# Optimization experiments

Measured on AMD Instinct MI355X. Metric: run time of the kernel, lower is better.

## Reference

```python
import jax, jax.numpy as jnp
import numpy as np

N, C, T, V, D = 64, 64, 256, 25, 64
BN_EPS = 1e-5


def _make_shift(v, ch, sign):
    idx = np.empty(v * ch, dtype=np.int64)
    for i in range(v):
        for j in range(ch):
            idx[i * ch + j] = (i * ch + j + sign * j * ch) % (ch * v)
    return jnp.asarray(idx, dtype=jnp.int32)


def setup_inputs() -> dict:
    key = jax.random.key(0)
    ks = jax.random.split(key, 8)
    return {
        "x0": jax.random.normal(ks[0], (N, C, T, V), dtype=jnp.float32),
        "fc1_w": jax.random.normal(ks[1], (C // 4, C), dtype=jnp.float32) * (1.0 / np.sqrt(C)),
        "fc1_b": jnp.zeros((C // 4,), dtype=jnp.float32),
        "fc2_w": jax.random.normal(ks[2], (4, C // 4), dtype=jnp.float32) * (1.0 / np.sqrt(C // 4)),
        "fc2_b": jnp.zeros((4,), dtype=jnp.float32),
        "Linear_weight": jax.random.normal(ks[3], (4, C, D), dtype=jnp.float32) * np.sqrt(1.0 / D),
        "Linear_bias": jax.random.normal(ks[4], (4, D), dtype=jnp.float32) * 0.02,
        "Feature_Mask": jax.random.normal(ks[5], (1, V, C), dtype=jnp.float32) * 0.1,
        "bn_gamma": 1.0 + 0.05 * jax.random.normal(ks[6], (V * D,), dtype=jnp.float32),
        "bn_beta": 0.05 * jax.random.normal(ks[7], (V * D,), dtype=jnp.float32),
        "shift_in": _make_shift(V, C, +1),
        "shift_out": _make_shift(V, D, -1),
        "epoch": 100,
    }


def reference(x0, fc1_w, fc1_b, fc2_w, fc2_b, Linear_weight, Linear_bias,
              Feature_Mask, bn_gamma, bn_beta, shift_in, shift_out, epoch):
    n, c, t, v = x0.shape
    d = Linear_weight.shape[-1]

    # DY_SEModule gate: global avg pool -> 1x1 convs -> tempered softmax over 4
    pooled = x0.mean(axis=(2, 3))                       # [n, c]
    h = jax.nn.relu(pooled @ fc1_w.T + fc1_b)           # [n, c//4]
    logits = h @ fc2_w.T + fc2_b                        # [n, 4]
    tao = (-(30.0 - 1.0) / 60.0 * epoch + 30.0) if epoch < 60 else 1.0
    gate = jax.nn.softmax(logits / tao, axis=1)         # [n, 4]

    # per-sample fused weights / bias
    W_fuse = jnp.einsum('kcd,nk->ncd', Linear_weight, gate)   # [n, c, d]
    b_fuse = jnp.einsum('kc,nk->nc', Linear_bias, gate)       # [n, d]

    # shift-in gather over flattened (v*c) channel axis
    x = x0.transpose(0, 2, 3, 1).reshape(n * t, v * c)  # [n*t, v*c]
    x = x[:, shift_in].reshape(n * t, v, c)
    x = x * (jnp.tanh(Feature_Mask) + 1.0)              # learnable feature mask
    x = x.reshape(n, t, v, c)

    # per-sample dynamic linear + bias
    x = jnp.einsum('ntvc,ncd->ntvd', x, W_fuse) + b_fuse[:, None, None, :]

    # shift-out gather
    x = x.reshape(n * t, v * d)[:, shift_out]           # [n*t, v*d]

    # BatchNorm1d (training mode: batch statistics over n*t)
    mean = x.mean(axis=0)
    var = jnp.var(x, axis=0)
    x = (x - mean) * jax.lax.rsqrt(var + BN_EPS) * bn_gamma + bn_beta

    x = x.reshape(n, t, v, d).transpose(0, 3, 1, 2)     # [n, d, t, v]
    return jax.nn.relu(x + x0)                          # identity residual (c == d)
```

## Files before the change

### kernel.cpp

```cpp
#include <hip/hip_runtime.h>
#include <hip/hip_bf16.h>
#include <math.h>

#define NN 64
#define CC 64
#define TT 256
#define VV 25
#define DD 64
#define BN_EPS 1e-5f

typedef short bf16x8 __attribute__((ext_vector_type(8)));
typedef float f32x4 __attribute__((ext_vector_type(4)));

#define WS_POOLED 0
#define WS_GATE   4096
#define WS_BFUSE  4352
#define WS_MASK   8448
#define WS_A      10048
#define WS_B      11648
#define WS_S1     13248
#define WS_S2     26048
#define WS_WTB    38848

#define OFF_W     0
#define OFF_MASK  9216
#define OFF_A     15728
#define OFF_B     22336
#define OFF_XM    28944
#define LDS_BYTES 54560

static __device__ __forceinline__ unsigned short f2bf(float x) {
    __hip_bfloat16 h = __float2bfloat16(x);
    return *(unsigned short*)&h;
}

__global__ __launch_bounds__(256) void k_pool(const float* __restrict__ x0,
                                              float* __restrict__ pooled) {
    __shared__ float red[256];
    const int bid = blockIdx.x;
    const float4* p = (const float4*)(x0 + (size_t)bid * (TT * VV));
    float s = 0.f;
    for (int k = threadIdx.x; k < (TT * VV) / 4; k += 256) {
        float4 v = p[k];
        s += v.x + v.y + v.z + v.w;
    }
    red[threadIdx.x] = s;
    __syncthreads();
    for (int off = 128; off > 0; off >>= 1) {
        if (threadIdx.x < off) red[threadIdx.x] += red[threadIdx.x + off];
        __syncthreads();
    }
    if (threadIdx.x == 0) pooled[bid] = red[0] * (1.f / (TT * VV));
}

__global__ __launch_bounds__(256) void k_gate(const float* __restrict__ fc1_w,
                                              const float* __restrict__ fc1_b,
                                              const float* __restrict__ fc2_w,
                                              const float* __restrict__ fc2_b,
                                              const float* __restrict__ lin_b,
                                              const float* __restrict__ fmask,
                                              const int* __restrict__ epoch_p,
                                              float* ws) {
    const int tid = threadIdx.x;
    float* pooled = ws + WS_POOLED;
    float* gate   = ws + WS_GATE;
    float* bfuse  = ws + WS_BFUSE;
    float* mask   = ws + WS_MASK;

    if (tid < 64) {
        const int n = tid;
        const float* po = pooled + n * 64;
        float h[16];
        for (int q = 0; q < 16; q++) {
            float z = fc1_b[q];
            for (int j = 0; j < 64; j++) z = fmaf(fc1_w[q * 64 + j], po[j], z);
            h[q] = fmaxf(z, 0.f);
        }
        float lg[4];
        for (int k = 0; k < 4; k++) {
            float z = fc2_b[k];
            for (int q = 0; q < 16; q++) z = fmaf(fc2_w[k * 16 + q], h[q], z);
            lg[k] = z;
        }
        const int ep = epoch_p[0];
        const float tao = (ep < 60) ? (-(29.0f / 60.0f) * (float)ep + 30.0f) : 1.0f;
        float mx = -1e30f;
        for (int k = 0; k < 4; k++) { lg[k] /= tao; mx = fmaxf(mx, lg[k]); }
        float se = 0.f;
        for (int k = 0; k < 4; k++) { lg[k] = expf(lg[k] - mx); se += lg[k]; }
        const float inv = 1.f / se;
        for (int k = 0; k < 4; k++) gate[n * 4 + k] = lg[k] * inv;
    }
    __syncthreads();
    for (int f = tid; f < 4096; f += 256) {
        const int n = f >> 6, d = f & 63;
        float s = 0.f;
        for (int k = 0; k < 4; k++) s = fmaf(lin_b[k * 64 + d], gate[n * 4 + k], s);
        bfuse[f] = s;
    }
    for (int f = tid; f < VV * CC; f += 256) mask[f] = tanhf(fmask[f]) + 1.0f;
}

__global__ __launch_bounds__(256) void k_wfuse(const float* __restrict__ lw, float* ws) {
    __shared__ float tile[64 * 65];
    const float* gate = ws + WS_GATE;
    unsigned short* wtb = (unsigned short*)(ws + WS_WTB);
    const int n = blockIdx.x;
    float g[4];
    for (int k = 0; k < 4; k++) g[k] = gate[n * 4 + k];
    for (int f = threadIdx.x; f < 4096; f += 256) {
        const int c = f >> 6, d = f & 63;
        float v = g[0] * lw[f] + g[1] * lw[4096 + f] + g[2] * lw[8192 + f] + g[3] * lw[12288 + f];
        tile[d * 65 + c] = v;
    }
    __syncthreads();
    for (int f = threadIdx.x; f < 4096; f += 256) {
        const int d = f >> 6, c = f & 63;
        wtb[n * 4096 + f] = f2bf(tile[d * 65 + c]);
    }
}

__global__ __launch_bounds__(256) void k_finalize(const float* __restrict__ gamma,
                                                  const float* __restrict__ beta,
                                                  float* ws) {
    const int f = blockIdx.x * 256 + threadIdx.x;
    if (f >= VV * DD) return;
    const int v = f >> 6, d = f & 63;
    const int vi = (v - d + 175) % 25;
    const int fin = vi * 64 + d;
    float s1 = 0.f, s2 = 0.f;
    for (int rep = 0; rep < 8; rep++) {
        s1 += ws[WS_S1 + rep * 1600 + fin];
        s2 += ws[WS_S2 + rep * 1600 + fin];
    }
    const float mean = s1 * (1.f / (NN * TT));
    float var = s2 * (1.f / (NN * TT)) - mean * mean;
    var = fmaxf(var, 0.f);
    const float rs = rsqrtf(var + BN_EPS);
    const float a = gamma[f] * rs;
    ws[WS_A + f] = a;
    ws[WS_B + f] = beta[f] - mean * a;
}

template <int PHASE>
__global__ __launch_bounds__(256) void k_main(const float* __restrict__ x0,
                                              const unsigned short* __restrict__ wtb,
                                              const float* __restrict__ ws,
                                              float* __restrict__ wsmut,
                                              float* __restrict__ out) {
    __shared__ __align__(16) char pool[LDS_BYTES];
    unsigned short (*Wl)[72] = (unsigned short(*)[72])(pool + OFF_W);
    float* maskL = (float*)(pool + OFF_MASK);
    float* Al = (float*)(pool + OFF_A);
    float* Bl = (float*)(pool + OFF_B);
    unsigned short (*Xm)[72] = (unsigned short(*)[72])(pool + OFF_XM);
    float* outl = (float*)(pool + OFF_XM);

    const int n = blockIdx.y, tb = blockIdx.x;
    const int tid = threadIdx.x;
    const int wv = tid >> 6, lane = tid & 63;
    const int lrow = lane & 15, lgrp = lane >> 4;
    const int dcol = wv * 16 + lrow;

    {
        const uint4* wsrc = (const uint4*)(wtb + n * 4096);
        for (int it = tid; it < 512; it += 256) {
            uint4 u = wsrc[it];
            const int f8 = it * 8;
            *(uint4*)&Wl[f8 >> 6][f8 & 63] = u;
        }
        const float* maskf = ws + WS_MASK;
        for (int f = tid; f < 1600; f += 256) {
            const int i = f >> 6, j = f & 63;
            maskL[i * 65 + j] = maskf[f];
        }
        if (PHASE == 0) {
            float* z = (float*)(pool + OFF_A);
            for (int f = tid; f < 3304; f += 256) z[f] = 0.f;
        } else {
            const float* Ag = ws + WS_A;
            const float* Bg = ws + WS_B;
            for (int f = tid; f < 1600; f += 256) {
                const int v = f >> 6, d = f & 63;
                Al[v * 66 + d] = Ag[f];
                Bl[v * 66 + d] = Bg[f];
            }
        }
    }
    const float bfv = ws[WS_BFUSE + n * 64 + dcol];
    __syncthreads();

    const bf16x8 b0 = *(const bf16x8*)&Wl[dcol][8 * lgrp];
    const bf16x8 b1 = *(const bf16x8*)&Wl[dcol][32 + 8 * lgrp];

    float s1r[7][4], s2r[7][4];
    if (PHASE == 0) {
#pragma unroll
        for (int m = 0; m < 7; m++)
#pragma unroll
            for (int r = 0; r < 4; r++) { s1r[m][r] = 0.f; s2r[m][r] = 0.f; }
    }

    const size_t nbase = (size_t)n * (CC * TT * VV);

    for (int ck = 0; ck < 4; ck++) {
        const int gcol0 = tb * 400 + ck * 100;
        for (int l4 = tid; l4 < 1600; l4 += 256) {
            const int j = l4 / 25, q = l4 - j * 25;
            const float4 xv = *(const float4*)(x0 + nbase + j * 6400 + gcol0 + q * 4);
            int jm = j; if (jm >= 50) jm -= 50; else if (jm >= 25) jm -= 25;
            const int r0 = q * 4;
            const float xe[4] = {xv.x, xv.y, xv.z, xv.w};
#pragma unroll
            for (int e = 0; e < 4; e++) {
                const int r = r0 + e;
                const int trel = (r >= 75) ? 3 : (r >= 50) ? 2 : (r >= 25) ? 1 : 0;
                const int p = r - trel * 25;
                int i = p - jm + 25; if (i >= 25) i -= 25;
                Xm[trel * 25 + i][j] = f2bf(xe[e] * maskL[i * 65 + j]);
            }
        }
        __syncthreads();
        f32x4 acc[7];
#pragma unroll
        for (int m = 0; m < 7; m++) {
            f32x4 a = {bfv, bfv, bfv, bfv};
            const bf16x8 a0 = *(const bf16x8*)&Xm[m * 16 + lrow][8 * lgrp];
            const bf16x8 a1 = *(const bf16x8*)&Xm[m * 16 + lrow][32 + 8 * lgrp];
            a = __builtin_amdgcn_mfma_f32_16x16x32_bf16(a0, b0, a, 0, 0, 0);
            a = __builtin_amdgcn_mfma_f32_16x16x32_bf16(a1, b1, a, 0, 0, 0);
            acc[m] = a;
        }
        __syncthreads();

        if (PHASE == 0) {
#pragma unroll
            for (int m = 0; m < 7; m++) {
#pragma unroll
                for (int r = 0; r < 4; r++) {
                    const int row = m * 16 + 4 * lgrp + r;
                    if (row < 100) {
                        const float y = acc[m][r];
                        s1r[m][r] += y;
                        s2r[m][r] = fmaf(y, y, s2r[m][r]);
                    }
                }
            }
        } else {
#pragma unroll
            for (int m = 0; m < 7; m++) {
#pragma unroll
                for (int r = 0; r < 4; r++) {
                    const int row = m * 16 + 4 * lgrp + r;
                    if (row < 100) {
                        const int trel = (row >= 75) ? 3 : (row >= 50) ? 2 : (row >= 25) ? 1 : 0;
                        const int v = row - trel * 25;
                        int vo = v + dcol;
                        if (vo >= 75) vo -= 75; else if (vo >= 50) vo -= 50; else if (vo >= 25) vo -= 25;
                        outl[dcol * 100 + trel * 25 + vo] =
                            fmaf(Al[vo * 66 + dcol], acc[m][r], Bl[vo * 66 + dcol]);
                    }
                }
            }
            __syncthreads();
            for (int l4 = tid; l4 < 1600; l4 += 256) {
                const int dd = l4 / 25, q = l4 - dd * 25;
                const float4 vv = *(const float4*)&outl[dd * 100 + q * 4];
                const float4 xr = *(const float4*)(x0 + nbase + dd * 6400 + gcol0 + q * 4);
                float4 o;
                o.x = fmaxf(vv.x + xr.x, 0.f);
                o.y = fmaxf(vv.y + xr.y, 0.f);
                o.z = fmaxf(vv.z + xr.z, 0.f);
                o.w = fmaxf(vv.w + xr.w, 0.f);
                *(float4*)(out + nbase + dd * 6400 + gcol0 + q * 4) = o;
            }
            __syncthreads();
        }
    }

    if (PHASE == 0) {
        float* s1l = Al;
        float* s2l = Bl;
#pragma unroll
        for (int m = 0; m < 7; m++) {
#pragma unroll
            for (int r = 0; r < 4; r++) {
                const int row = m * 16 + 4 * lgrp + r;
                if (row < 100) {
                    int v = row;
                    if (v >= 75) v -= 75; else if (v >= 50) v -= 50; else if (v >= 25) v -= 25;
                    __hip_atomic_fetch_add(&s1l[v * 66 + dcol], s1r[m][r],
                                           __ATOMIC_RELAXED, __HIP_MEMORY_SCOPE_WORKGROUP);
                    __hip_atomic_fetch_add(&s2l[v * 66 + dcol], s2r[m][r],
                                           __ATOMIC_RELAXED, __HIP_MEMORY_SCOPE_WORKGROUP);
                }
            }
        }
        __syncthreads();
        float* g1 = wsmut + WS_S1 + (n & 7) * 1600;
        float* g2 = wsmut + WS_S2 + (n & 7) * 1600;
        for (int f = tid; f < 1600; f += 256) {
            const int v = f >> 6, d = f & 63;
            atomicAdd(&g1[f], s1l[v * 66 + d]);
            atomicAdd(&g2[f], s2l[v * 66 + d]);
        }
    }
}

extern "C" void kernel_launch(void* const* d_in, const int* in_sizes, int n_in,
                              void* d_out, int out_size, void* d_ws, size_t ws_size,
                              hipStream_t stream) {
    const float* x0    = (const float*)d_in[0];
    const float* fc1_w = (const float*)d_in[1];
    const float* fc1_b = (const float*)d_in[2];
    const float* fc2_w = (const float*)d_in[3];
    const float* fc2_b = (const float*)d_in[4];
    const float* lw    = (const float*)d_in[5];
    const float* lb    = (const float*)d_in[6];
    const float* fmask = (const float*)d_in[7];
    const float* gamma = (const float*)d_in[8];
    const float* beta  = (const float*)d_in[9];
    const int* epoch   = (const int*)d_in[12];
    float* ws  = (float*)d_ws;
    float* out = (float*)d_out;
    const unsigned short* wtb = (const unsigned short*)(ws + WS_WTB);

    k_pool<<<NN * CC, 256, 0, stream>>>(x0, ws + WS_POOLED);
    k_gate<<<1, 256, 0, stream>>>(fc1_w, fc1_b, fc2_w, fc2_b, lb, fmask, epoch, ws);
    k_wfuse<<<NN, 256, 0, stream>>>(lw, ws);
    hipMemsetAsync((char*)d_ws + WS_S1 * sizeof(float), 0, 25600 * sizeof(float), stream);

    dim3 g2(16, 64);
    k_main<0><<<g2, 256, 0, stream>>>(x0, wtb, ws, ws, out);
    k_finalize<<<7, 256, 0, stream>>>(gamma, beta, ws);
    k_main<1><<<g2, 256, 0, stream>>>(x0, wtb, ws, ws, out);
}
```

Before: 230.4 us.

## Shrink LDS, double phase-1 grid, write output directly from MFMA registers

Phase 1 now computes the transposed MFMA product (W as A operand) and writes the normalized, residual-added output straight from registers instead of staging through LDS, which drops two barriers per chunk. BN scale and shift are packed as a bf16 pair in one word, LDS is sized per phase with a launch bound of 4 blocks per CU, phase 1 uses twice as many blocks, and atomic stat replicas grow from 8 to 16. The goals are higher occupancy, less LDS traffic and sync, and less atomic contention. The costs are bf16 rounding of the BN scale and shift, and scattered, uncoalesced scalar global loads and stores in the epilogue.

```diff
diff --git a/kernel.cpp b/kernel.cpp
--- a/kernel.cpp
+++ b/kernel.cpp
@@ -8,6 +8,7 @@
 #define VV 25
 #define DD 64
 #define BN_EPS 1e-5f
+#define NREP 16
 
 typedef short bf16x8 __attribute__((ext_vector_type(8)));
 typedef float f32x4 __attribute__((ext_vector_type(4)));
@@ -16,18 +17,10 @@
 #define WS_GATE   4096
 #define WS_BFUSE  4352
 #define WS_MASK   8448
-#define WS_A      10048
-#define WS_B      11648
+#define WS_ABP    10048
 #define WS_S1     13248
-#define WS_S2     26048
-#define WS_WTB    38848
-
-#define OFF_W     0
-#define OFF_MASK  9216
-#define OFF_A     15728
-#define OFF_B     22336
-#define OFF_XM    28944
-#define LDS_BYTES 54560
+#define WS_S2     38848
+#define WS_WTB    64448
 
 static __device__ __forceinline__ unsigned short f2bf(float x) {
     __hip_bfloat16 h = __float2bfloat16(x);
@@ -129,7 +122,7 @@
     const int vi = (v - d + 175) % 25;
     const int fin = vi * 64 + d;
     float s1 = 0.f, s2 = 0.f;
-    for (int rep = 0; rep < 8; rep++) {
+    for (int rep = 0; rep < NREP; rep++) {
         s1 += ws[WS_S1 + rep * 1600 + fin];
         s2 += ws[WS_S2 + rep * 1600 + fin];
     }
@@ -138,29 +131,32 @@
     var = fmaxf(var, 0.f);
     const float rs = rsqrtf(var + BN_EPS);
     const float a = gamma[f] * rs;
-    ws[WS_A + f] = a;
-    ws[WS_B + f] = beta[f] - mean * a;
+    const float b = beta[f] - mean * a;
+    const unsigned pa = (unsigned)f2bf(a);
+    const unsigned pb = (unsigned)f2bf(b);
+    ((unsigned*)ws)[WS_ABP + f] = pa | (pb << 16);
 }
 
 template <int PHASE>
-__global__ __launch_bounds__(256) void k_main(const float* __restrict__ x0,
-                                              const unsigned short* __restrict__ wtb,
-                                              const float* __restrict__ ws,
-                                              float* __restrict__ wsmut,
-                                              float* __restrict__ out) {
-    __shared__ __align__(16) char pool[LDS_BYTES];
-    unsigned short (*Wl)[72] = (unsigned short(*)[72])(pool + OFF_W);
-    float* maskL = (float*)(pool + OFF_MASK);
-    float* Al = (float*)(pool + OFF_A);
-    float* Bl = (float*)(pool + OFF_B);
-    unsigned short (*Xm)[72] = (unsigned short(*)[72])(pool + OFF_XM);
-    float* outl = (float*)(pool + OFF_XM);
+__global__ __launch_bounds__(256, 4) void k_main(const float* __restrict__ x0,
+                                                 const unsigned short* __restrict__ wtb,
+                                                 const float* __restrict__ ws,
+                                                 float* __restrict__ wsmut,
+                                                 float* __restrict__ out) {
+    constexpr int LDSZ = (PHASE == 0) ? 31856 : 38656;
+    __shared__ __align__(16) char pool[LDSZ];
+    unsigned short (*Wl)[72] = (unsigned short(*)[72])(pool);
+    float* maskL = (float*)(pool + 9216);
+    unsigned short (*Xm)[72] = (unsigned short(*)[72])(pool + 15728);
+    unsigned* ABl = (unsigned*)(pool + 31856);
 
     const int n = blockIdx.y, tb = blockIdx.x;
     const int tid = threadIdx.x;
     const int wv = tid >> 6, lane = tid & 63;
     const int lrow = lane & 15, lgrp = lane >> 4;
     const int dcol = wv * 16 + lrow;
+    constexpr int NCK = (PHASE == 0) ? 4 : 2;
+    const int colbase = tb * 100 * NCK;
 
     {
         const uint4* wsrc = (const uint4*)(wtb + n * 4096);
@@ -169,29 +165,25 @@
             const int f8 = it * 8;
             *(uint4*)&Wl[f8 >> 6][f8 & 63] = u;
         }
-        const float* maskf = ws + WS_MASK;
-        for (int f = tid; f < 1600; f += 256) {
-            const int i = f >> 6, j = f & 63;
-            maskL[i * 65 + j] = maskf[f];
-        }
-        if (PHASE == 0) {
-            float* z = (float*)(pool + OFF_A);
-            for (int f = tid; f < 3304; f += 256) z[f] = 0.f;
-        } else {
-            const float* Ag = ws + WS_A;
-            const float* Bg = ws + WS_B;
-            for (int f = tid; f < 1600; f += 256) {
-                const int v = f >> 6, d = f & 63;
-                Al[v * 66 + d] = Ag[f];
-                Bl[v * 66 + d] = Bg[f];
-            }
+        for (int f = tid; f < 1600; f += 256)
+            maskL[(f >> 6) * 65 + (f & 63)] = ws[WS_MASK + f];
+        for (int f = tid; f < 864; f += 256) ((unsigned short*)Xm)[7200 + f] = 0;
+        if (PHASE == 1) {
+            const unsigned* abp = (const unsigned*)(ws + WS_ABP);
+            for (int f = tid; f < 1600; f += 256)
+                ABl[(f >> 6) * 68 + (f & 63)] = abp[f];
         }
     }
     const float bfv = ws[WS_BFUSE + n * 64 + dcol];
+    f32x4 bias4;
+    if (PHASE == 1) {
+        const float4 b4 = *(const float4*)&ws[WS_BFUSE + n * 64 + wv * 16 + 4 * lgrp];
+        bias4[0] = b4.x; bias4[1] = b4.y; bias4[2] = b4.z; bias4[3] = b4.w;
+    }
     __syncthreads();
 
-    const bf16x8 b0 = *(const bf16x8*)&Wl[dcol][8 * lgrp];
-    const bf16x8 b1 = *(const bf16x8*)&Wl[dcol][32 + 8 * lgrp];
+    const bf16x8 w0 = *(const bf16x8*)&Wl[dcol][8 * lgrp];
+    const bf16x8 w1 = *(const bf16x8*)&Wl[dcol][32 + 8 * lgrp];
 
     float s1r[7][4], s2r[7][4];
     if (PHASE == 0) {
@@ -203,84 +195,86 @@
 
     const size_t nbase = (size_t)n * (CC * TT * VV);
 
-    for (int ck = 0; ck < 4; ck++) {
-        const int gcol0 = tb * 400 + ck * 100;
+    for (int ck = 0; ck < NCK; ck++) {
+        const int gcol0 = colbase + ck * 100;
+        if (ck) __syncthreads();
         for (int l4 = tid; l4 < 1600; l4 += 256) {
             const int j = l4 / 25, q = l4 - j * 25;
             const float4 xv = *(const float4*)(x0 + nbase + j * 6400 + gcol0 + q * 4);
             int jm = j; if (jm >= 50) jm -= 50; else if (jm >= 25) jm -= 25;
-            const int r0 = q * 4;
             const float xe[4] = {xv.x, xv.y, xv.z, xv.w};
 #pragma unroll
             for (int e = 0; e < 4; e++) {
-                const int r = r0 + e;
+                const int r = q * 4 + e;
                 const int trel = (r >= 75) ? 3 : (r >= 50) ? 2 : (r >= 25) ? 1 : 0;
                 const int p = r - trel * 25;
-                int i = p - jm + 25; if (i >= 25) i -= 25;
+                int i = p - jm; if (i < 0) i += 25;
                 Xm[trel * 25 + i][j] = f2bf(xe[e] * maskL[i * 65 + j]);
             }
         }
         __syncthreads();
-        f32x4 acc[7];
-#pragma unroll
-        for (int m = 0; m < 7; m++) {
-            f32x4 a = {bfv, bfv, bfv, bfv};
-            const bf16x8 a0 = *(const bf16x8*)&Xm[m * 16 + lrow][8 * lgrp];
-            const bf16x8 a1 = *(const bf16x8*)&Xm[m * 16 + lrow][32 + 8 * lgrp];
-            a = __builtin_amdgcn_mfma_f32_16x16x32_bf16(a0, b0, a, 0, 0, 0);
-            a = __builtin_amdgcn_mfma_f32_16x16x32_bf16(a1, b1, a, 0, 0, 0);
-            acc[m] = a;
-        }
-        __syncthreads();
 
         if (PHASE == 0) {
 #pragma unroll
             for (int m = 0; m < 7; m++) {
+                f32x4 a = {bfv, bfv, bfv, bfv};
+                const bf16x8 a0 = *(const bf16x8*)&Xm[m * 16 + lrow][8 * lgrp];
+                const bf16x8 a1 = *(const bf16x8*)&Xm[m * 16 + lrow][32 + 8 * lgrp];
+                a = __builtin_amdgcn_mfma_f32_16x16x32_bf16(a0, w0, a, 0, 0, 0);
+                a = __builtin_amdgcn_mfma_f32_16x16x32_bf16(a1, w1, a, 0, 0, 0);
 #pragma unroll
                 for (int r = 0; r < 4; r++) {
                     const int row = m * 16 + 4 * lgrp + r;
                     if (row < 100) {
-                        const float y = acc[m][r];
+                        const float y = a[r];
                         s1r[m][r] += y;
                         s2r[m][r] = fmaf(y, y, s2r[m][r]);
                     }
                 }
             }
         } else {
-#pragma unroll
-            for (int m = 0; m < 7; m++) {
-#pragma unroll
-                for (int r = 0; r < 4; r++) {
-                    const int row = m * 16 + 4 * lgrp + r;
-                    if (row < 100) {
-                        const int trel = (row >= 75) ? 3 : (row >= 50) ? 2 : (row >= 25) ? 1 : 0;
-                        const int v = row - trel * 25;
-                        int vo = v + dcol;
+            f32x4 acc[7];
+#pragma unroll
+            for (int tvt = 0; tvt < 7; tvt++) {
+                f32x4 a = bias4;
+                const bf16x8 xb0 = *(const bf16x8*)&Xm[tvt * 16 + lrow][8 * lgrp];
+                const bf16x8 xb1 = *(const bf16x8*)&Xm[tvt * 16 + lrow][32 + 8 * lgrp];
+                a = __builtin_amdgcn_mfma_f32_16x16x32_bf16(w0, xb0, a, 0, 0, 0);
+                a = __builtin_amdgcn_mfma_f32_16x16x32_bf16(w1, xb1, a, 0, 0, 0);
+                acc[tvt] = a;
+            }
+            const int dB = wv * 16 + 4 * lgrp;
+#pragma unroll
+            for (int tvt = 0; tvt < 7; tvt++) {
+                const int rloc = tvt * 16 + lrow;
+                if (rloc < 100) {
+                    const int grow = gcol0 + rloc;
+                    const int t = grow / 25;
+                    const int v = grow - t * 25;
+                    const int vv0 = v + dB;
+#pragma unroll
+                    for (int r = 0; r < 4; r++) {
+                        int vo = vv0 + r;
                         if (vo >= 75) vo -= 75; else if (vo >= 50) vo -= 50; else if (vo >= 25) vo -= 25;
-                        outl[dcol * 100 + trel * 25 + vo] =
-                            fmaf(Al[vo * 66 + dcol], acc[m][r], Bl[vo * 66 + dcol]);
+                        const int d = dB + r;
+                        const unsigned u = ABl[vo * 68 + d];
+                        const float a_ = __uint_as_float(u << 16);
+                        const float b_ = __uint_as_float(u & 0xffff0000u);
+                        const size_t off = nbase + (size_t)d * 6400 + t * 25 + vo;
+                        const float val = fmaf(a_, acc[tvt][r], b_) + x0[off];
+                        out[off] = fmaxf(val, 0.f);
                     }
                 }
             }
-            __syncthreads();
-            for (int l4 = tid; l4 < 1600; l4 += 256) {
-                const int dd = l4 / 25, q = l4 - dd * 25;
-                const float4 vv = *(const float4*)&outl[dd * 100 + q * 4];
-                const float4 xr = *(const float4*)(x0 + nbase + dd * 6400 + gcol0 + q * 4);
-                float4 o;
-                o.x = fmaxf(vv.x + xr.x, 0.f);
-                o.y = fmaxf(vv.y + xr.y, 0.f);
-                o.z = fmaxf(vv.z + xr.z, 0.f);
-                o.w = fmaxf(vv.w + xr.w, 0.f);
-                *(float4*)(out + nbase + dd * 6400 + gcol0 + q * 4) = o;
-            }
-            __syncthreads();
         }
     }
 
     if (PHASE == 0) {
-        float* s1l = Al;
-        float* s2l = Bl;
+        __syncthreads();
+        float* s1l = (float*)(pool + 15728);
+        float* s2l = s1l + 1650;
+        for (int f = tid; f < 3300; f += 256) s1l[f] = 0.f;
+        __syncthreads();
 #pragma unroll
         for (int m = 0; m < 7; m++) {
 #pragma unroll
@@ -297,12 +291,12 @@
             }
         }
         __syncthreads();
-        float* g1 = wsmut + WS_S1 + (n & 7) * 1600;
-        float* g2 = wsmut + WS_S2 + (n & 7) * 1600;
+        const int rep = (n * 5 + tb) & (NREP - 1);
+        float* g1 = wsmut + WS_S1 + rep * 1600;
+        float* g2 = wsmut + WS_S2 + rep * 1600;
         for (int f = tid; f < 1600; f += 256) {
-            const int v = f >> 6, d = f & 63;
-            atomicAdd(&g1[f], s1l[v * 66 + d]);
-            atomicAdd(&g2[f], s2l[v * 66 + d]);
+            atomicAdd(&g1[f], s1l[(f >> 6) * 66 + (f & 63)]);
+            atomicAdd(&g2[f], s2l[(f >> 6) * 66 + (f & 63)]);
         }
     }
 }
@@ -328,10 +322,9 @@
     k_pool<<<NN * CC, 256, 0, stream>>>(x0, ws + WS_POOLED);
     k_gate<<<1, 256, 0, stream>>>(fc1_w, fc1_b, fc2_w, fc2_b, lb, fmask, epoch, ws);
     k_wfuse<<<NN, 256, 0, stream>>>(lw, ws);
-    hipMemsetAsync((char*)d_ws + WS_S1 * sizeof(float), 0, 25600 * sizeof(float), stream);
-
-    dim3 g2(16, 64);
-    k_main<0><<<g2, 256, 0, stream>>>(x0, wtb, ws, ws, out);
+    hipMemsetAsync((char*)d_ws + WS_S1 * sizeof(float), 0, (size_t)NREP * 3200 * sizeof(float), stream);
+
+    k_main<0><<<dim3(16, 64), 256, 0, stream>>>(x0, wtb, ws, ws, out);
     k_finalize<<<7, 256, 0, stream>>>(gamma, beta, ws);
-    k_main<1><<<g2, 256, 0, stream>>>(x0, wtb, ws, ws, out);
-}
+    k_main<1><<<dim3(32, 64), 256, 0, stream>>>(x0, wtb, ws, ws, out);
+}
```

New measurement: 271.3 us. 17.7% more time.
